# Performance work log

Hardware: AMD Instinct MI355X
Metric: run time of the kernel (lower is better)

## Reference

```python
import jax, jax.numpy as jnp
import numpy as np


def setup_inputs() -> dict:
    key = jax.random.key(0)
    k1, k2, k3 = jax.random.split(key, 3)
    B, L, H, E = 2, 2048, 16, 64
    queries = jax.random.normal(k1, (B, L, H, E), dtype=jnp.float32)
    keys = jax.random.normal(k2, (B, L, H, E), dtype=jnp.float32)
    values = jax.random.normal(k3, (B, L, H, E), dtype=jnp.float32)
    a1 = jnp.ones((), dtype=jnp.float32)
    a2 = jnp.ones((), dtype=jnp.float32)
    return {"queries": queries, "keys": keys, "values": values, "a1": a1, "a2": a2}


def reference(queries, keys, values, a1, a2):
    # ASSAAttention forward (eval mode: dropout is identity)
    B, L, H, E = queries.shape
    scale = 1.0 / jnp.sqrt(jnp.asarray(E, queries.dtype))
    # shared QK scores: [B, H, L, S]
    qk_scores = jnp.einsum('blhe,bshe->bhls', queries, keys) * scale
    # sparse path: squared-ReLU weighting
    ssa_scores = jax.nn.relu(qk_scores) ** 2
    ssa_output = jnp.einsum('bhls,bshd->blhd', ssa_scores, values)
    # dense path: softmax weighting
    dsa_scores = jax.nn.softmax(qk_scores, axis=-1)
    dsa_output = jnp.einsum('bhls,bshd->blhd', dsa_scores, values)
    # scalar blend with softmax over (a1, a2)
    w1 = jnp.exp(a1)
    w2 = jnp.exp(a2)
    alpha1 = w1 / (w1 + w2)
    alpha2 = w2 / (w1 + w2)
    return alpha1 * ssa_output + alpha2 * dsa_output
```

## Files before the change

kernel.cpp:

```cpp
#include <hip/hip_runtime.h>
#include <hip/hip_bf16.h>

typedef __attribute__((ext_vector_type(8))) short short8;
typedef __attribute__((ext_vector_type(4))) float f32x4;
typedef __attribute__((ext_vector_type(4))) unsigned uint4v;

#define LOG2E 1.4426950408889634f
#define ILN2SQ 0.4804530139182014f

__device__ __forceinline__ unsigned packbf2(float a, float b) {
  __hip_bfloat162 h = __float22bfloat162_rn(make_float2(a, b));
  return *reinterpret_cast<unsigned*>(&h);
}
__device__ __forceinline__ int swz(int row) {
  return ((row & 7) << 4) ^ (((row >> 3) & 3) << 5);
}
__device__ __forceinline__ void gload16(const void* g, void* l) {
  __builtin_amdgcn_global_load_lds(
      (const __attribute__((address_space(1))) unsigned int*)g,
      (__attribute__((address_space(3))) unsigned int*)l, 16, 0, 0);
}

__device__ __forceinline__ int pv_key(int p) {
  const int R = p >> 5, g = (p & 31) >> 3, jj = p & 7;
  return (R * 2 + (jj >> 2)) * 16 + g * 4 + (jj & 3);
}

__global__ __launch_bounds__(256) void assa_prep(
    const float* __restrict__ K, const float* __restrict__ V, char* __restrict__ WS)
{
  constexpr int L = 2048, RS = 1024, E = 64;
  char* KP = WS;
  char* VTP = WS + (size_t)8 * 1024 * 1024;
  __shared__ float tile[64][65];
  const int tid = threadIdx.x;

  if (blockIdx.x < 1024) {
    const int gid = blockIdx.x * 256 + tid;
    const int rid = gid >> 2;
    const int e0 = (gid & 3) * 16;
    const int bh = rid >> 11, s = rid & 2047;
    const int b = bh >> 4, h = bh & 15;
    const float* kr = K + ((size_t)b * L + s) * RS + h * E + e0;
    const float4 u0 = *(const float4*)(kr);
    const float4 u1 = *(const float4*)(kr + 4);
    const float4 u2 = *(const float4*)(kr + 8);
    const float4 u3 = *(const float4*)(kr + 12);
    uint4v w0, w1;
    w0[0] = packbf2(u0.x, u0.y); w0[1] = packbf2(u0.z, u0.w);
    w0[2] = packbf2(u1.x, u1.y); w0[3] = packbf2(u1.z, u1.w);
    w1[0] = packbf2(u2.x, u2.y); w1[1] = packbf2(u2.z, u2.w);
    w1[2] = packbf2(u3.x, u3.y); w1[3] = packbf2(u3.z, u3.w);
    char* dst = KP + (size_t)rid * 128;
    const int sz = swz(s);
    *(uint4v*)(dst + ((e0 * 2) ^ sz)) = w0;
    *(uint4v*)(dst + ((e0 * 2 + 16) ^ sz)) = w1;
  } else {
    const int bx = blockIdx.x - 1024;
    const int bh = bx >> 5, t5 = bx & 31;
    const int b = bh >> 4, h = bh & 15;
    const float* vb = V + ((size_t)b * L + t5 * 64) * RS + h * E;
    {
      const int key = tid >> 2, e0 = (tid & 3) * 16;
      const float* vr = vb + (size_t)key * RS + e0;
      const float4 u0 = *(const float4*)(vr);
      const float4 u1 = *(const float4*)(vr + 4);
      const float4 u2 = *(const float4*)(vr + 8);
      const float4 u3 = *(const float4*)(vr + 12);
      float* tr = &tile[key][e0];
      tr[0] = u0.x; tr[1] = u0.y; tr[2] = u0.z; tr[3] = u0.w;
      tr[4] = u1.x; tr[5] = u1.y; tr[6] = u1.z; tr[7] = u1.w;
      tr[8] = u2.x; tr[9] = u2.y; tr[10] = u2.z; tr[11] = u2.w;
      tr[12] = u3.x; tr[13] = u3.y; tr[14] = u3.z; tr[15] = u3.w;
    }
    __syncthreads();
    const int e = tid >> 2, p0 = (tid & 3) * 16;
    uint4v w0, w1;
    #pragma unroll
    for (int i = 0; i < 4; ++i)
      w0[i] = packbf2(tile[pv_key(p0 + 2 * i)][e], tile[pv_key(p0 + 2 * i + 1)][e]);
    #pragma unroll
    for (int i = 0; i < 4; ++i)
      w1[i] = packbf2(tile[pv_key(p0 + 8 + 2 * i)][e], tile[pv_key(p0 + 9 + 2 * i)][e]);
    char* dst = VTP + ((size_t)bx * 64 + e) * 128;
    const int sz = swz(e);
    *(uint4v*)(dst + ((p0 * 2) ^ sz)) = w0;
    *(uint4v*)(dst + ((p0 * 2 + 16) ^ sz)) = w1;
  }
}

__global__ __launch_bounds__(512, 4) void assa_fused(
    const float* __restrict__ Q, const char* __restrict__ WS,
    const float* __restrict__ A1, const float* __restrict__ A2,
    float* __restrict__ O)
{
  constexpr int L = 2048, H = 16, E = 64, RS = H * E;

  __shared__ __align__(16) char Kb[2 * 8192];
  __shared__ __align__(16) char Vb[2 * 8192];

  const int t = threadIdx.x;
  const int wv = t >> 6;
  const int lane = t & 63;
  const int g = lane >> 4;
  const int c = lane & 15;

  const int bh = blockIdx.x;
  const int q0 = blockIdx.y * 128;
  const int b = bh >> 4;
  const int h = bh & 15;

  const float* qb = Q + (size_t)b * L * RS + (size_t)h * E;
  float* ob = O + (size_t)b * L * RS + (size_t)h * E;
  const char* KP = WS;
  const char* VTP = WS + (size_t)8 * 1024 * 1024;

  const float a1 = A1[0], a2 = A2[0];
  const float am = fmaxf(a1, a2);
  const float e1 = expf(a1 - am), e2 = expf(a2 - am);
  const float alpha1 = (e1 / (e1 + e2)) * ILN2SQ;
  const float alpha2 = e2 / (e1 + e2);

  short8 aq[2];
  {
    const float qs = 0.125f * LOG2E;
    const float* qr = qb + (size_t)(q0 + wv * 16 + c) * RS;
    #pragma unroll
    for (int ks = 0; ks < 2; ++ks) {
      const float4 u0 = *(const float4*)(qr + ks * 32 + g * 8);
      const float4 u1 = *(const float4*)(qr + ks * 32 + g * 8 + 4);
      union { unsigned u[4]; short8 s; } f;
      f.u[0] = packbf2(u0.x * qs, u0.y * qs);
      f.u[1] = packbf2(u0.z * qs, u0.w * qs);
      f.u[2] = packbf2(u1.x * qs, u1.y * qs);
      f.u[3] = packbf2(u1.z * qs, u1.w * qs);
      aq[ks] = f.s;
    }
  }

  int ka[8];
  #pragma unroll
  for (int kt = 0; kt < 4; ++kt) {
    const int row = kt * 16 + c;
    const int s = swz(row);
    ka[kt * 2 + 0] = (row * 128 + g * 16) ^ s;
    ka[kt * 2 + 1] = (row * 128 + 64 + g * 16) ^ s;
  }
  int va[8];
  #pragma unroll
  for (int et = 0; et < 4; ++et) {
    const int row = et * 16 + c;
    const int s = swz(row);
    va[et * 2 + 0] = (row * 128 + g * 16) ^ s;
    va[et * 2 + 1] = (row * 128 + 64 + g * 16) ^ s;
  }

  const f32x4 zero4 = {0.0f, 0.0f, 0.0f, 0.0f};
  f32x4 od[4], os[4];
  #pragma unroll
  for (int i = 0; i < 4; ++i) { od[i] = zero4; os[i] = zero4; }
  float psum = 0.0f;

  const char* kp = KP + (size_t)bh * (2048 * 128) + t * 16;
  const char* vp = VTP + (size_t)bh * (2048 * 128) + t * 16;
  char* kd = Kb + wv * 1024 + lane * 16 - lane * 16;
  char* vd = Vb + wv * 1024 + lane * 16 - lane * 16;

  union U8 { unsigned u[4]; short8 s; };

#define STAGE(TOFF, HALF)                              \
  do {                                                 \
    gload16(kp + (TOFF), kd + (HALF));                 \
    gload16(vp + (TOFF), vd + (HALF));                 \
  } while (0)

#define PROC(ACC, OD, OS, PSUM)                                                      \
  do {                                                                               \
    unsigned pdw[8], psw[8];                                                         \
    _Pragma("unroll")                                                                \
    for (int kt = 0; kt < 4; ++kt) {                                                 \
      const float x0 = __builtin_amdgcn_exp2f(ACC[kt][0]);                           \
      const float x1 = __builtin_amdgcn_exp2f(ACC[kt][1]);                           \
      const float x2 = __builtin_amdgcn_exp2f(ACC[kt][2]);                           \
      const float x3 = __builtin_amdgcn_exp2f(ACC[kt][3]);                           \
      PSUM += (x0 + x1) + (x2 + x3);                                                 \
      const float r0 = fmaxf(ACC[kt][0], 0.0f), r1 = fmaxf(ACC[kt][1], 0.0f);        \
      const float r2 = fmaxf(ACC[kt][2], 0.0f), r3 = fmaxf(ACC[kt][3], 0.0f);        \
      pdw[kt * 2 + 0] = packbf2(x0, x1);                                             \
      pdw[kt * 2 + 1] = packbf2(x2, x3);                                             \
      psw[kt * 2 + 0] = packbf2(r0 * r0, r1 * r1);                                   \
      psw[kt * 2 + 1] = packbf2(r2 * r2, r3 * r3);                                   \
    }                                                                                \
    _Pragma("unroll")                                                                \
    for (int tp = 0; tp < 2; ++tp) {                                                 \
      U8 bpd, bps;                                                                   \
      bpd.u[0] = pdw[tp * 4 + 0]; bpd.u[1] = pdw[tp * 4 + 1];                        \
      bpd.u[2] = pdw[tp * 4 + 2]; bpd.u[3] = pdw[tp * 4 + 3];                        \
      bps.u[0] = psw[tp * 4 + 0]; bps.u[1] = psw[tp * 4 + 1];                        \
      bps.u[2] = psw[tp * 4 + 2]; bps.u[3] = psw[tp * 4 + 3];                        \
      _Pragma("unroll")                                                              \
      for (int et = 0; et < 4; ++et) {                                               \
        const short8 vf = tp ? vfr1[et] : vfr0[et];                                  \
        OD[et] = __builtin_amdgcn_mfma_f32_16x16x32_bf16(vf, bpd.s, OD[et], 0, 0, 0);\
        OS[et] = __builtin_amdgcn_mfma_f32_16x16x32_bf16(vf, bps.s, OS[et], 0, 0, 0);\
      }                                                                              \
    }                                                                                \
  } while (0)

#define COMPUTE(OFS)                                                                 \
  do {                                                                               \
    f32x4 acc[4];                                                                    \
    _Pragma("unroll")                                                                \
    for (int i = 0; i < 4; ++i) acc[i] = zero4;                                      \
    _Pragma("unroll")                                                                \
    for (int kt = 0; kt < 4; ++kt) {                                                 \
      const short8 kf0 = *(const short8*)(Kb + ka[kt * 2 + 0] + (OFS));              \
      const short8 kf1 = *(const short8*)(Kb + ka[kt * 2 + 1] + (OFS));              \
      acc[kt] = __builtin_amdgcn_mfma_f32_16x16x32_bf16(kf0, aq[0], acc[kt], 0, 0, 0);\
      acc[kt] = __builtin_amdgcn_mfma_f32_16x16x32_bf16(kf1, aq[1], acc[kt], 0, 0, 0);\
    }                                                                                \
    short8 vfr0[4], vfr1[4];                                                         \
    _Pragma("unroll")                                                                \
    for (int et = 0; et < 4; ++et) {                                                 \
      vfr0[et] = *(const short8*)(Vb + va[et * 2 + 0] + (OFS));                      \
      vfr1[et] = *(const short8*)(Vb + va[et * 2 + 1] + (OFS));                      \
    }                                                                                \
    PROC(acc, od, os, psum);                                                         \
  } while (0)

  STAGE(0, 0);
  __syncthreads();
  size_t toff = 8192;
  for (int it = 0; it < 32; it += 2) {
    STAGE(toff, 8192); toff += 8192;
    COMPUTE(0);
    __syncthreads();
    if (it + 2 < 32) { STAGE(toff, 0); toff += 8192; }
    COMPUTE(8192);
    __syncthreads();
  }
#undef STAGE
#undef PROC
#undef COMPUTE

  float l = psum;
  l += __shfl_xor(l, 16);
  l += __shfl_xor(l, 32);

  const float wd = alpha2 / l;
  float* orow = ob + (size_t)(q0 + wv * 16 + c) * RS;
  #pragma unroll
  for (int et = 0; et < 4; ++et) {
    float4 o;
    o.x = alpha1 * os[et][0] + wd * od[et][0];
    o.y = alpha1 * os[et][1] + wd * od[et][1];
    o.z = alpha1 * os[et][2] + wd * od[et][2];
    o.w = alpha1 * os[et][3] + wd * od[et][3];
    *(float4*)(orow + et * 16 + g * 4) = o;
  }
}

extern "C" void kernel_launch(void* const* d_in, const int* in_sizes, int n_in,
                              void* d_out, int out_size, void* d_ws, size_t ws_size,
                              hipStream_t stream) {
  const float* q = (const float*)d_in[0];
  const float* k = (const float*)d_in[1];
  const float* v = (const float*)d_in[2];
  const float* a1 = (const float*)d_in[3];
  const float* a2 = (const float*)d_in[4];
  float* out = (float*)d_out;
  char* ws = (char*)d_ws;

  assa_prep<<<2048, 256, 0, stream>>>(k, v, ws);
  dim3 grid(32, 16);
  assa_fused<<<grid, 512, 0, stream>>>(q, ws, a1, a2, out);
}
```

Baseline: 77.17 us.

## Double the K/V stage size and batch QK MFMAs ahead of softmax-PV

```diff
diff --git a/kernel.cpp b/kernel.cpp
--- a/kernel.cpp
+++ b/kernel.cpp
@@ -96,8 +96,8 @@
 {
   constexpr int L = 2048, H = 16, E = 64, RS = H * E;
 
-  __shared__ __align__(16) char Kb[2 * 8192];
-  __shared__ __align__(16) char Vb[2 * 8192];
+  __shared__ __align__(16) char Kb[2 * 16384];
+  __shared__ __align__(16) char Vb[2 * 16384];
 
   const int t = threadIdx.x;
   const int wv = t >> 6;
@@ -163,19 +163,38 @@
 
   const char* kp = KP + (size_t)bh * (2048 * 128) + t * 16;
   const char* vp = VTP + (size_t)bh * (2048 * 128) + t * 16;
-  char* kd = Kb + wv * 1024 + lane * 16 - lane * 16;
-  char* vd = Vb + wv * 1024 + lane * 16 - lane * 16;
+  char* kd = Kb + wv * 1024;
+  char* vd = Vb + wv * 1024;
 
   union U8 { unsigned u[4]; short8 s; };
 
-#define STAGE(TOFF, HALF)                              \
-  do {                                                 \
-    gload16(kp + (TOFF), kd + (HALF));                 \
-    gload16(vp + (TOFF), vd + (HALF));                 \
+#define STAGE(TOFF, HALF)                                \
+  do {                                                   \
+    gload16(kp + (TOFF), kd + (HALF));                   \
+    gload16(kp + (TOFF) + 8192, kd + (HALF) + 8192);     \
+    gload16(vp + (TOFF), vd + (HALF));                   \
+    gload16(vp + (TOFF) + 8192, vd + (HALF) + 8192);     \
   } while (0)
 
-#define PROC(ACC, OD, OS, PSUM)                                                      \
+#define QKPART(ACC, OFS)                                                             \
   do {                                                                               \
+    _Pragma("unroll")                                                                \
+    for (int kt = 0; kt < 4; ++kt) {                                                 \
+      const short8 kf0 = *(const short8*)(Kb + ka[kt * 2 + 0] + (OFS));              \
+      const short8 kf1 = *(const short8*)(Kb + ka[kt * 2 + 1] + (OFS));              \
+      ACC[kt] = __builtin_amdgcn_mfma_f32_16x16x32_bf16(kf0, aq[0], ACC[kt], 0, 0, 0);\
+      ACC[kt] = __builtin_amdgcn_mfma_f32_16x16x32_bf16(kf1, aq[1], ACC[kt], 0, 0, 0);\
+    }                                                                                \
+  } while (0)
+
+#define SMPV(ACC, OFS)                                                               \
+  do {                                                                               \
+    short8 vfr0[4], vfr1[4];                                                         \
+    _Pragma("unroll")                                                                \
+    for (int et = 0; et < 4; ++et) {                                                 \
+      vfr0[et] = *(const short8*)(Vb + va[et * 2 + 0] + (OFS));                      \
+      vfr1[et] = *(const short8*)(Vb + va[et * 2 + 1] + (OFS));                      \
+    }                                                                                \
     unsigned pdw[8], psw[8];                                                         \
     _Pragma("unroll")                                                                \
     for (int kt = 0; kt < 4; ++kt) {                                                 \
@@ -183,7 +202,7 @@
       const float x1 = __builtin_amdgcn_exp2f(ACC[kt][1]);                           \
       const float x2 = __builtin_amdgcn_exp2f(ACC[kt][2]);                           \
       const float x3 = __builtin_amdgcn_exp2f(ACC[kt][3]);                           \
-      PSUM += (x0 + x1) + (x2 + x3);                                                 \
+      psum += (x0 + x1) + (x2 + x3);                                                 \
       const float r0 = fmaxf(ACC[kt][0], 0.0f), r1 = fmaxf(ACC[kt][1], 0.0f);        \
       const float r2 = fmaxf(ACC[kt][2], 0.0f), r3 = fmaxf(ACC[kt][3], 0.0f);        \
       pdw[kt * 2 + 0] = packbf2(x0, x1);                                             \
@@ -191,6 +210,7 @@
       psw[kt * 2 + 0] = packbf2(r0 * r0, r1 * r1);                                   \
       psw[kt * 2 + 1] = packbf2(r2 * r2, r3 * r3);                                   \
     }                                                                                \
+    __builtin_amdgcn_s_setprio(1);                                                   \
     _Pragma("unroll")                                                                \
     for (int tp = 0; tp < 2; ++tp) {                                                 \
       U8 bpd, bps;                                                                   \
@@ -201,47 +221,31 @@
       _Pragma("unroll")                                                              \
       for (int et = 0; et < 4; ++et) {                                               \
         const short8 vf = tp ? vfr1[et] : vfr0[et];                                  \
-        OD[et] = __builtin_amdgcn_mfma_f32_16x16x32_bf16(vf, bpd.s, OD[et], 0, 0, 0);\
-        OS[et] = __builtin_amdgcn_mfma_f32_16x16x32_bf16(vf, bps.s, OS[et], 0, 0, 0);\
+        od[et] = __builtin_amdgcn_mfma_f32_16x16x32_bf16(vf, bpd.s, od[et], 0, 0, 0);\
+        os[et] = __builtin_amdgcn_mfma_f32_16x16x32_bf16(vf, bps.s, os[et], 0, 0, 0);\
       }                                                                              \
     }                                                                                \
-  } while (0)
-
-#define COMPUTE(OFS)                                                                 \
-  do {                                                                               \
-    f32x4 acc[4];                                                                    \
-    _Pragma("unroll")                                                                \
-    for (int i = 0; i < 4; ++i) acc[i] = zero4;                                      \
-    _Pragma("unroll")                                                                \
-    for (int kt = 0; kt < 4; ++kt) {                                                 \
-      const short8 kf0 = *(const short8*)(Kb + ka[kt * 2 + 0] + (OFS));              \
-      const short8 kf1 = *(const short8*)(Kb + ka[kt * 2 + 1] + (OFS));              \
-      acc[kt] = __builtin_amdgcn_mfma_f32_16x16x32_bf16(kf0, aq[0], acc[kt], 0, 0, 0);\
-      acc[kt] = __builtin_amdgcn_mfma_f32_16x16x32_bf16(kf1, aq[1], acc[kt], 0, 0, 0);\
-    }                                                                                \
-    short8 vfr0[4], vfr1[4];                                                         \
-    _Pragma("unroll")                                                                \
-    for (int et = 0; et < 4; ++et) {                                                 \
-      vfr0[et] = *(const short8*)(Vb + va[et * 2 + 0] + (OFS));                      \
-      vfr1[et] = *(const short8*)(Vb + va[et * 2 + 1] + (OFS));                      \
-    }                                                                                \
-    PROC(acc, od, os, psum);                                                         \
+    __builtin_amdgcn_s_setprio(0);                                                   \
   } while (0)
 
   STAGE(0, 0);
   __syncthreads();
-  size_t toff = 8192;
-  for (int it = 0; it < 32; it += 2) {
-    STAGE(toff, 8192); toff += 8192;
-    COMPUTE(0);
+  size_t toff = 16384;
+  for (int r = 0; r < 16; ++r) {
+    if (r + 1 < 16) { STAGE(toff, ((r + 1) & 1) * 16384); toff += 16384; }
+    const int OFS = (r & 1) * 16384;
+    f32x4 acc0[4], acc1[4];
+    #pragma unroll
+    for (int i = 0; i < 4; ++i) { acc0[i] = zero4; acc1[i] = zero4; }
+    QKPART(acc0, OFS);
+    QKPART(acc1, OFS + 8192);
+    SMPV(acc0, OFS);
+    SMPV(acc1, OFS + 8192);
     __syncthreads();
-    if (it + 2 < 32) { STAGE(toff, 0); toff += 8192; }
-    COMPUTE(8192);
-    __syncthreads();
   }
 #undef STAGE
-#undef PROC
-#undef COMPUTE
+#undef QKPART
+#undef SMPV
 
   float l = psum;
   l += __shfl_xor(l, 16);
```

Result: slower. 90.43 us (+17.2%).
